# Optimization experiments

Hardware: AMD Instinct MI355X
Metric: run time of the kernel (lower is better)

## Reference

```python
import jax, jax.numpy as jnp
from jax import lax
import numpy as np

V, E, H, L = 32000, 512, 1024, 2
B, S, T = 32, 128, 128
PAD = 0


def _lstm_step(h, c, gates):
    i, f, g, o = jnp.split(gates, 4, axis=-1)
    c_new = jax.nn.sigmoid(f) * c + jax.nn.sigmoid(i) * jnp.tanh(g)
    h_new = jax.nn.sigmoid(o) * jnp.tanh(c_new)
    return h_new, c_new


def _lstm_layer(x_tbe, Wih, Whh, bih, bhh):
    # x_tbe: [T, B, in]; returns hs [T, B, H], final (h, c)
    Bn = x_tbe.shape[1]
    Hn = Whh.shape[1]
    h0 = jnp.zeros((Bn, Hn), x_tbe.dtype)
    c0 = jnp.zeros((Bn, Hn), x_tbe.dtype)

    def step(carry, x_t):
        h, c = carry
        gates = x_t @ Wih.T + h @ Whh.T + (bih + bhh)
        h, c = _lstm_step(h, c, gates)
        return (h, c), h

    (h, c), hs = lax.scan(step, (h0, c0), x_tbe)
    return hs, h, c


def setup_inputs() -> dict:
    key = jax.random.key(0)
    ks = iter(jax.random.split(key, 32))
    s = 0.02

    def p(shape):
        return (jax.random.normal(next(ks), shape, dtype=jnp.float32) * s)

    embed = p((V, E)).at[PAD].set(0.0)  # padding_idx row zeroed
    inp = {
        'src': jax.random.randint(next(ks), (B, S), 0, V),
        'tgt': jax.random.randint(next(ks), (B, T), 0, V),
        'embed': embed,
        'enc_Wih0': p((4 * H, E)), 'enc_Whh0': p((4 * H, H)),
        'enc_bih0': p((4 * H,)), 'enc_bhh0': p((4 * H,)),
        'enc_Wih1': p((4 * H, H)), 'enc_Whh1': p((4 * H, H)),
        'enc_bih1': p((4 * H,)), 'enc_bhh1': p((4 * H,)),
        'dec_Wih': p((4 * H, E + H)), 'dec_Whh': p((4 * H, H)),
        'dec_bih': p((4 * H,)), 'dec_bhh': p((4 * H,)),
        'fc_W': p((V, H)), 'fc_b': p((V,)),
    }
    return inp


def reference(src, tgt, embed, enc_Wih0, enc_Whh0, enc_bih0, enc_bhh0,
              enc_Wih1, enc_Whh1, enc_bih1, enc_bhh1,
              dec_Wih, dec_Whh, dec_bih, dec_bhh, fc_W, fc_b):
    # ----- encoder: 2-layer LSTM -----
    enc_emb = embed[src]                       # [B, S, E]
    x = jnp.transpose(enc_emb, (1, 0, 2))      # [S, B, E]
    hs0, _, _ = _lstm_layer(x, enc_Wih0, enc_Whh0, enc_bih0, enc_bhh0)
    hs1, h_last, c_last = _lstm_layer(hs0, enc_Wih1, enc_Whh1, enc_bih1, enc_bhh1)
    enc_out = jnp.transpose(hs1, (1, 0, 2))    # [B, S, H]

    # ----- decoder: attention + LSTMCell per step -----
    dec_emb = embed[tgt[:, :-1]]               # inputs for steps 1..T-1: [B, T-1, E]
    dec_xs = jnp.transpose(dec_emb, (1, 0, 2)) # [T-1, B, E]

    def dec_step(carry, x_t):
        h, c = carry
        scores = jnp.einsum('bsh,bh->bs', enc_out, h)
        w = jax.nn.softmax(scores, axis=1)
        ctx = jnp.einsum('bs,bsh->bh', w, enc_out)
        xin = jnp.concatenate([x_t, ctx], axis=1)   # [B, E+H]
        gates = xin @ dec_Wih.T + h @ dec_Whh.T + (dec_bih + dec_bhh)
        h, c = _lstm_step(h, c, gates)
        out = h @ fc_W.T + fc_b                     # [B, V]
        return (h, c), out

    _, outs = lax.scan(dec_step, (h_last, c_last), dec_xs)  # [T-1, B, V]
    return jnp.transpose(outs, (1, 0, 2))                   # [B, T-1, V]
```

## Files before the change

### kernel.cpp

```cpp
#include <hip/hip_runtime.h>

typedef unsigned short u16;
typedef __bf16 bf16x8 __attribute__((ext_vector_type(8)));
typedef float f32x4 __attribute__((ext_vector_type(4)));
typedef u16 u16x8 __attribute__((ext_vector_type(8)));
typedef unsigned u32x2 __attribute__((ext_vector_type(2)));

static_assert(sizeof(bf16x8) == 16, "bf16x8 must be 16B");

#define DEV static __device__ __forceinline__

DEV u16 f2bf(float f) {
  unsigned u = __float_as_uint(f);
  u += 0x7FFFu + ((u >> 16) & 1u);
  return (u16)(u >> 16);
}
DEV float bf2f(u16 h) { return __uint_as_float(((unsigned)h) << 16); }
DEV f32x4 mfma16(bf16x8 a, bf16x8 b, f32x4 c) {
  return __builtin_amdgcn_mfma_f32_16x16x32_bf16(a, b, c, 0, 0, 0);
}
DEV bf16x8 ldfrag(const u16* p) { return *reinterpret_cast<const bf16x8*>(p); }
DEV float sigf(float x) { return 1.0f / (1.0f + __expf(-x)); }
DEV bf16x8 asbf(f32x4 v) { union { f32x4 f; bf16x8 h; } u; u.f = v; return u.h; }
DEV void gld16(const void* g, void* l) {
  __builtin_amdgcn_global_load_lds((const __attribute__((address_space(1))) void*)g,
                                   (__attribute__((address_space(3))) void*)l, 16, 0, 0);
}

DEV void ld_a16_coh(const void* p0, const void* p1,
                    f32x4& a0, f32x4& a1, f32x4& a2, f32x4& a3,
                    f32x4& a4, f32x4& a5, f32x4& a6, f32x4& a7,
                    f32x4& b0, f32x4& b1, f32x4& b2, f32x4& b3,
                    f32x4& b4, f32x4& b5, f32x4& b6, f32x4& b7) {
  asm volatile(
      "global_load_dwordx4 %0, %16, off sc0 sc1\n\t"
      "global_load_dwordx4 %1, %16, off offset:64 sc0 sc1\n\t"
      "global_load_dwordx4 %2, %16, off offset:128 sc0 sc1\n\t"
      "global_load_dwordx4 %3, %16, off offset:192 sc0 sc1\n\t"
      "global_load_dwordx4 %4, %16, off offset:256 sc0 sc1\n\t"
      "global_load_dwordx4 %5, %16, off offset:320 sc0 sc1\n\t"
      "global_load_dwordx4 %6, %16, off offset:384 sc0 sc1\n\t"
      "global_load_dwordx4 %7, %16, off offset:448 sc0 sc1\n\t"
      "global_load_dwordx4 %8, %17, off sc0 sc1\n\t"
      "global_load_dwordx4 %9, %17, off offset:64 sc0 sc1\n\t"
      "global_load_dwordx4 %10, %17, off offset:128 sc0 sc1\n\t"
      "global_load_dwordx4 %11, %17, off offset:192 sc0 sc1\n\t"
      "global_load_dwordx4 %12, %17, off offset:256 sc0 sc1\n\t"
      "global_load_dwordx4 %13, %17, off offset:320 sc0 sc1\n\t"
      "global_load_dwordx4 %14, %17, off offset:384 sc0 sc1\n\t"
      "global_load_dwordx4 %15, %17, off offset:448 sc0 sc1\n\t"
      "s_waitcnt vmcnt(0)"
      : "=&v"(a0), "=&v"(a1), "=&v"(a2), "=&v"(a3), "=&v"(a4), "=&v"(a5), "=&v"(a6), "=&v"(a7),
        "=&v"(b0), "=&v"(b1), "=&v"(b2), "=&v"(b3), "=&v"(b4), "=&v"(b5), "=&v"(b6), "=&v"(b7)
      : "v"(p0), "v"(p1)
      : "memory");
}
DEV void ld_a16_coh_nw(const void* p0, const void* p1,
                       f32x4& a0, f32x4& a1, f32x4& a2, f32x4& a3,
                       f32x4& a4, f32x4& a5, f32x4& a6, f32x4& a7,
                       f32x4& b0, f32x4& b1, f32x4& b2, f32x4& b3,
                       f32x4& b4, f32x4& b5, f32x4& b6, f32x4& b7) {
  asm volatile(
      "global_load_dwordx4 %0, %16, off sc0 sc1\n\t"
      "global_load_dwordx4 %1, %16, off offset:64 sc0 sc1\n\t"
      "global_load_dwordx4 %2, %16, off offset:128 sc0 sc1\n\t"
      "global_load_dwordx4 %3, %16, off offset:192 sc0 sc1\n\t"
      "global_load_dwordx4 %4, %16, off offset:256 sc0 sc1\n\t"
      "global_load_dwordx4 %5, %16, off offset:320 sc0 sc1\n\t"
      "global_load_dwordx4 %6, %16, off offset:384 sc0 sc1\n\t"
      "global_load_dwordx4 %7, %16, off offset:448 sc0 sc1\n\t"
      "global_load_dwordx4 %8, %17, off sc0 sc1\n\t"
      "global_load_dwordx4 %9, %17, off offset:64 sc0 sc1\n\t"
      "global_load_dwordx4 %10, %17, off offset:128 sc0 sc1\n\t"
      "global_load_dwordx4 %11, %17, off offset:192 sc0 sc1\n\t"
      "global_load_dwordx4 %12, %17, off offset:256 sc0 sc1\n\t"
      "global_load_dwordx4 %13, %17, off offset:320 sc0 sc1\n\t"
      "global_load_dwordx4 %14, %17, off offset:384 sc0 sc1\n\t"
      "global_load_dwordx4 %15, %17, off offset:448 sc0 sc1"
      : "=&v"(a0), "=&v"(a1), "=&v"(a2), "=&v"(a3), "=&v"(a4), "=&v"(a5), "=&v"(a6), "=&v"(a7),
        "=&v"(b0), "=&v"(b1), "=&v"(b2), "=&v"(b3), "=&v"(b4), "=&v"(b5), "=&v"(b6), "=&v"(b7)
      : "v"(p0), "v"(p1)
      : "memory");
}
DEV f32x4 ld16_coh(const void* p) {
  f32x4 r;
  asm volatile("global_load_dwordx4 %0, %1, off sc0 sc1\n\ts_waitcnt vmcnt(0)"
               : "=&v"(r) : "v"(p) : "memory");
  return r;
}
DEV void ld32_coh(const void* p, f32x4& a, f32x4& b) {
  asm volatile(
      "global_load_dwordx4 %0, %2, off sc0 sc1\n\t"
      "global_load_dwordx4 %1, %2, off offset:16 sc0 sc1\n\t"
      "s_waitcnt vmcnt(0)"
      : "=&v"(a), "=&v"(b) : "v"(p) : "memory");
}
DEV void st32_coh(void* p, unsigned v) {
  asm volatile("global_store_dword %0, %1, off sc0 sc1" ::"v"(p), "v"(v) : "memory");
}
DEV void st8_coh(void* p, unsigned lo, unsigned hi) {
  u32x2 v; v[0] = lo; v[1] = hi;
  asm volatile("global_store_dwordx2 %0, %1, off sc0 sc1" ::"v"(p), "v"(v) : "memory");
}

DEV unsigned ldflag(const unsigned* p) {
  unsigned r;
  asm volatile("global_load_dword %0, %1, off sc0 sc1\n\ts_waitcnt vmcnt(0)"
               : "=&v"(r) : "v"(p) : "memory");
  return r;
}
DEV void poll128(const unsigned* fl, unsigned tgt) {
  if (tgt == 0) return;
  if (threadIdx.x < 64) {
    const unsigned* p0 = fl + (size_t)threadIdx.x * 16;
    const unsigned* p1 = fl + (size_t)(threadIdx.x + 64) * 16;
    for (;;) {
      unsigned a, b;
      asm volatile(
          "global_load_dword %0, %2, off sc0 sc1\n\t"
          "global_load_dword %1, %3, off sc0 sc1\n\t"
          "s_waitcnt vmcnt(0)"
          : "=&v"(a), "=&v"(b) : "v"(p0), "v"(p1) : "memory");
      if (__all((a >= tgt) && (b >= tgt))) break;
      __builtin_amdgcn_s_sleep(1);
    }
  }
  __syncthreads();
}
DEV void poll32(const unsigned* fl, unsigned tgt) {
  if (threadIdx.x < 64) {
    const unsigned* p0 = fl + (size_t)(threadIdx.x & 31) * 16;
    for (;;) {
      unsigned a = ldflag(p0);
      if (__all(a >= tgt)) break;
      __builtin_amdgcn_s_sleep(1);
    }
  }
  __syncthreads();
}
DEV void pollAB(const unsigned* f0, unsigned t0, const unsigned* f1, unsigned t1) {
  const bool n0 = t0 > 0, n1 = t1 > 0;
  if ((n0 || n1) && threadIdx.x < 64) {
    const unsigned* q0 = f0 + (size_t)threadIdx.x * 16;
    const unsigned* q1 = f0 + (size_t)(threadIdx.x + 64) * 16;
    const unsigned* q2 = f1 + (size_t)threadIdx.x * 16;
    const unsigned* q3 = f1 + (size_t)(threadIdx.x + 64) * 16;
    for (;;) {
      unsigned a, b, c, d;
      asm volatile(
          "global_load_dword %0, %4, off sc0 sc1\n\t"
          "global_load_dword %1, %5, off sc0 sc1\n\t"
          "global_load_dword %2, %6, off sc0 sc1\n\t"
          "global_load_dword %3, %7, off sc0 sc1\n\t"
          "s_waitcnt vmcnt(0)"
          : "=&v"(a), "=&v"(b), "=&v"(c), "=&v"(d)
          : "v"(q0), "v"(q1), "v"(q2), "v"(q3) : "memory");
      bool ok = true;
      if (n0) ok = ok && (a >= t0) && (b >= t0);
      if (n1) ok = ok && (c >= t1) && (d >= t1);
      if (__all(ok)) break;
      __builtin_amdgcn_s_sleep(1);
    }
  }
  __syncthreads();
}
DEV void setflag(unsigned* f, unsigned v) {
  asm volatile("s_waitcnt vmcnt(0)" ::: "memory");
  __syncthreads();
  if (threadIdx.x == 0) st32_coh(f, v);
}

#define Bn 32
#define Sn 128
#define Td 127
#define En 512
#define Hn 1024
#define G4 4096
#define Vn 32000

typedef u16 u16x8b __attribute__((ext_vector_type(8)));
__global__ __launch_bounds__(256) void cvt_bf16_kernel(const float* __restrict__ in,
                                                       u16* __restrict__ out, int n8) {
  int gid = blockIdx.x * 256 + threadIdx.x;
  if (gid >= n8) return;
  const float4* ip = (const float4*)in + gid * 2;
  float4 x = ip[0], y = ip[1];
  u16x8b o;
  o[0] = f2bf(x.x); o[1] = f2bf(x.y); o[2] = f2bf(x.z); o[3] = f2bf(x.w);
  o[4] = f2bf(y.x); o[5] = f2bf(y.y); o[6] = f2bf(y.z); o[7] = f2bf(y.w);
  ((u16x8b*)out)[gid] = o;
}

__global__ __launch_bounds__(256) void gather_embed_kernel(const int* __restrict__ idx, int ldidx,
                                                           const float* __restrict__ embed,
                                                           u16* __restrict__ outA, int nrows) {
  int gid = blockIdx.x * 256 + threadIdx.x;
  int total = nrows * (En / 8);
  if (gid >= total) return;
  int r = gid / (En / 8);
  int ck = gid % (En / 8);
  int tcol = r / Bn, b = r % Bn;
  int tok = idx[b * ldidx + tcol];
  const float4* src = (const float4*)(embed + (size_t)tok * En + ck * 8);
  float4 x = src[0], y = src[1];
  u16x8b o;
  o[0] = f2bf(x.x); o[1] = f2bf(x.y); o[2] = f2bf(x.z); o[3] = f2bf(x.w);
  o[4] = f2bf(y.x); o[5] = f2bf(y.y); o[6] = f2bf(y.z); o[7] = f2bf(y.w);
  *(u16x8b*)(outA + (size_t)r * En + ck * 8) = o;
}

__global__ __launch_bounds__(256) void gemm_tile_kernel(const u16* __restrict__ A, int lda,
                                                        const u16* __restrict__ W, int ldw,
                                                        const float* __restrict__ bias0,
                                                        const float* __restrict__ bias1,
                                                        float* __restrict__ Cout, int ldc,
                                                        int Mtiles, int K, int mode) {
  __shared__ u16 Asb[128 * 32];
  __shared__ u16 Bsb[128 * 32];
  int nwg = gridDim.x;
  int cpx = nwg >> 3;
  int bid = ((int)blockIdx.x & 7) * cpx + ((int)blockIdx.x >> 3);
  int mt = bid % Mtiles, nt = bid / Mtiles;
  int tid = threadIdx.x;
  int wave = tid >> 6, lane = tid & 63;
  int lrow = lane & 15, kgrp = lane >> 4;
  int wr = wave >> 1, wc = wave & 1;
  int e0 = wave * 1024 + lane * 8;
  int r0 = e0 >> 5, c0 = e0 & 31;
  int r1 = r0 + 16;
  const u16* Ab = A + (size_t)(mt * 128) * lda;
  const u16* Wb = W + (size_t)(nt * 128) * ldw;
  u16* AsW = Asb + wave * 1024;
  u16* BsW = Bsb + wave * 1024;
  f32x4 acc[4][4] = {};
  for (int k0 = 0; k0 < K; k0 += 32) {
    gld16(Ab + (size_t)r0 * lda + k0 + c0, AsW);
    gld16(Ab + (size_t)r1 * lda + k0 + c0, AsW + 512);
    gld16(Wb + (size_t)r0 * ldw + k0 + c0, BsW);
    gld16(Wb + (size_t)r1 * ldw + k0 + c0, BsW + 512);
    __syncthreads();
    bf16x8 af[4], bfr[4];
#pragma unroll
    for (int i = 0; i < 4; ++i) af[i] = ldfrag(Asb + (wr * 64 + i * 16 + lrow) * 32 + kgrp * 8);
#pragma unroll
    for (int i = 0; i < 4; ++i) bfr[i] = ldfrag(Bsb + (wc * 64 + i * 16 + lrow) * 32 + kgrp * 8);
#pragma unroll
    for (int i = 0; i < 4; ++i)
#pragma unroll
      for (int j = 0; j < 4; ++j) acc[i][j] = mfma16(af[i], bfr[j], acc[i][j]);
    __syncthreads();
  }
  if (mode == 0) {
#pragma unroll
    for (int i = 0; i < 4; ++i) {
      int m = mt * 128 + wr * 64 + i * 16 + kgrp * 4;
#pragma unroll
      for (int j = 0; j < 4; ++j) {
        int n = nt * 128 + wc * 64 + j * 16 + lrow;
        float bb = (bias0 ? bias0[n] : 0.f) + (bias1 ? bias1[n] : 0.f);
#pragma unroll
        for (int r = 0; r < 4; ++r) Cout[(size_t)(m + r) * ldc + n] = acc[i][j][r] + bb;
      }
    }
  } else {
#pragma unroll
    for (int i = 0; i < 4; ++i) {
      int m = mt * 128 + wr * 64 + i * 16 + kgrp * 4;
#pragma unroll
      for (int j = 0; j < 4; ++j) {
        int n = nt * 128 + wc * 64 + j * 16 + lrow;
        float bb = bias0[n];
#pragma unroll
        for (int r = 0; r < 4; ++r) {
          int mm = m + r;
          if (mm < Td * Bn) {
            int tt = mm >> 5, b = mm & 31;
            Cout[((size_t)b * Td + tt) * Vn + n] = acc[i][j][r] + bb;
          }
        }
      }
    }
  }
}

DEV void mm8b(const u16* __restrict__ A0, const char* __restrict__ Wl, int pitchB,
              int kByteBase, int lane, f32x4 acc[2][2]) {
  const int lrow = lane & 15, kgrp = lane >> 4;
  const char* wr0 = Wl + (size_t)lrow * pitchB;
  const char* wr1 = wr0 + (size_t)16 * pitchB;
  const int sw = (lrow & 7) << 4;
  f32x4 s0, s1, s2, s3, s4, s5, s6, s7, u0, u1, u2, u3, u4, u5, u6, u7;
  ld_a16_coh(A0 + (size_t)lrow * 1024 + kgrp * 8, A0 + (size_t)(16 + lrow) * 1024 + kgrp * 8,
             s0, s1, s2, s3, s4, s5, s6, s7, u0, u1, u2, u3, u4, u5, u6, u7);
#define KS(T, U, J, KB)                                                \
  {                                                                    \
    bf16x8 a = asbf(T);                                                \
    int kb = (KB) + (J) * 64 + kgrp * 16;                              \
    bf16x8 w0 = *(const bf16x8*)(wr0 + (size_t)(kb ^ sw));             \
    bf16x8 w1 = *(const bf16x8*)(wr1 + (size_t)(kb ^ sw));             \
    acc[0][0] = mfma16(a, w0, acc[0][0]);                              \
    acc[0][1] = mfma16(a, w1, acc[0][1]);                              \
    bf16x8 cc = asbf(U);                                               \
    acc[1][0] = mfma16(cc, w0, acc[1][0]);                             \
    acc[1][1] = mfma16(cc, w1, acc[1][1]);                             \
  }
  KS(s0, u0, 0, kByteBase) KS(s1, u1, 1, kByteBase) KS(s2, u2, 2, kByteBase)
  KS(s3, u3, 3, kByteBase) KS(s4, u4, 4, kByteBase) KS(s5, u5, 5, kByteBase)
  KS(s6, u6, 6, kByteBase) KS(s7, u7, 7, kByteBase)
}

DEV void mm8b_pair(const u16* __restrict__ A0, const char* __restrict__ Wl, int pitchB,
                   int kByteBase, int lane, f32x4 acc[2][2]) {
  const int lrow = lane & 15, kgrp = lane >> 4;
  const char* wr0 = Wl + (size_t)lrow * pitchB;
  const char* wr1 = wr0 + (size_t)16 * pitchB;
  const int sw = (lrow & 7) << 4;
  f32x4 s0, s1, s2, s3, s4, s5, s6, s7, u0, u1, u2, u3, u4, u5, u6, u7;
  f32x4 t0, t1, t2, t3, t4, t5, t6, t7, v0, v1, v2, v3, v4, v5, v6, v7;
  ld_a16_coh_nw(A0 + (size_t)lrow * 1024 + kgrp * 8, A0 + (size_t)(16 + lrow) * 1024 + kgrp * 8,
                s0, s1, s2, s3, s4, s5, s6, s7, u0, u1, u2, u3, u4, u5, u6, u7);
  ld_a16_coh(A0 + (size_t)lrow * 1024 + 256 + kgrp * 8,
             A0 + (size_t)(16 + lrow) * 1024 + 256 + kgrp * 8,
             t0, t1, t2, t3, t4, t5, t6, t7, v0, v1, v2, v3, v4, v5, v6, v7);
  __builtin_amdgcn_sched_barrier(0);
  KS(s0, u0, 0, kByteBase) KS(s1, u1, 1, kByteBase) KS(s2, u2, 2, kByteBase)
  KS(s3, u3, 3, kByteBase) KS(s4, u4, 4, kByteBase) KS(s5, u5, 5, kByteBase)
  KS(s6, u6, 6, kByteBase) KS(s7, u7, 7, kByteBase)
  KS(t0, v0, 0, kByteBase + 512) KS(t1, v1, 1, kByteBase + 512) KS(t2, v2, 2, kByteBase + 512)
  KS(t3, v3, 3, kByteBase + 512) KS(t4, v4, 4, kByteBase + 512) KS(t5, v5, 5, kByteBase + 512)
  KS(t6, v6, 6, kByteBase + 512) KS(t7, v7, 7, kByteBase + 512)
}

DEV void dump_acc(float* red, f32x4 acc[2][2], int wave, int lane) {
  int lrow = lane & 15, kgrp = lane >> 4;
#pragma unroll
  for (int m = 0; m < 2; ++m)
#pragma unroll
    for (int n = 0; n < 2; ++n)
#pragma unroll
      for (int r = 0; r < 4; ++r)
        red[((((wave * 2 + m) * 2 + n) * 16) + kgrp * 4 + r) * 16 + lrow] = acc[m][n][r];
}
DEV float rsum(const float* red, int m, int n, int rw, int l) {
  float s = 0.f;
#pragma unroll
  for (int w = 0; w < 4; ++w) s += red[((((w * 2 + m) * 2 + n) * 16) + rw) * 16 + l];
  return s;
}
DEV float lstm_apply(const float gs[4], float* c_reg) {
  float ig = sigf(gs[0]), fg = sigf(gs[1]), gg = tanhf(gs[2]), og = sigf(gs[3]);
  float cn = fg * (*c_reg) + ig * gg;
  *c_reg = cn;
  return og * tanhf(cn);
}

__global__ __launch_bounds__(256, 1) void enc_persist9(
    const float* __restrict__ premix, const u16* __restrict__ Whh0, const u16* __restrict__ Wih1,
    const u16* __restrict__ Whh1, const float* __restrict__ bih1, const float* __restrict__ bhh1,
    u16* __restrict__ h0ring, u16* __restrict__ h1ring, float* __restrict__ c1_out,
    u16* __restrict__ enc_b, unsigned* __restrict__ f0, unsigned* __restrict__ f1) {
  extern __shared__ char lds[];
  float* red = (float*)(lds + 131072);
  const int tid = threadIdx.x, wave = tid >> 6, lane = tid & 63;
  const int blk = blockIdx.x;
  const bool l1 = blk >= 128;
  const int base = (blk & 127) * 8;
  if (!l1) {
    for (int i = tid; i < 4096; i += 256) {
      int c = i >> 7;
      int kb = (i & 127) << 4;
      int row = (c >> 3) * Hn + base + (c & 7);
      f32x4 v = *(const f32x4*)(Whh0 + (size_t)row * Hn + (kb >> 1));
      *(f32x4*)(lds + c * 2048 + (kb ^ ((c & 7) << 4))) = v;
    }
  } else {
    for (int i = tid; i < 8192; i += 256) {
      int c = i >> 8;
      int kb = (i & 255) << 4;
      int row = (c >> 3) * Hn + base + (c & 7);
      const u16* src = (kb < 2048) ? (Wih1 + (size_t)row * Hn + (kb >> 1))
                                   : (Whh1 + (size_t)row * Hn + ((kb - 2048) >> 1));
      f32x4 v = *(const f32x4*)src;
      *(f32x4*)(lds + c * 4096 + (kb ^ ((c & 7) << 4))) = v;
    }
  }
  const int b_ = tid >> 3, hc = tid & 7;
  const int m = b_ >> 4, rw = b_ & 15;
  const size_t off = (size_t)b_ * Hn + base + hc;
  float c_reg = 0.f;
  __syncthreads();
  if (!l1) {
    for (int i = 0; i < Sn; ++i) {
      const float* pmr = premix + (size_t)i * (Bn * G4) + (size_t)b_ * G4 + base + hc;
      float pmv[4];
#pragma unroll
      for (int g = 0; g < 4; ++g) pmv[g] = pmr[(size_t)g * Hn];
      pollAB(f0, (unsigned)i, f1, (i >= 3) ? (unsigned)(i - 2) : 0u);
      const u16* hin = h0ring + (size_t)(i & 3) * (Bn * Hn);
      f32x4 acc[2][2] = {};
      mm8b(hin + wave * 256, lds, 2048, wave * 512, lane, acc);
      dump_acc(red, acc, wave, lane);
      __syncthreads();
      float gs[4];
#pragma unroll
      for (int g = 0; g < 4; ++g) {
        int c = g * 8 + hc;
        gs[g] = rsum(red, m, c >> 4, rw, c & 15) + pmv[g];
      }
      float hn = lstm_apply(gs, &c_reg);
      u16 mine = f2bf(hn);
      unsigned nb = (unsigned)(u16)__shfl_xor((int)mine, 1);
      if (!(tid & 1))
        st32_coh(h0ring + (size_t)((i + 1) & 3) * (Bn * Hn) + off,
                 ((unsigned)mine) | (nb << 16));
      setflag(f0 + blk * 16, (unsigned)(i + 1));
    }
  } else {
    float badd[4];
#pragma unroll
    for (int g = 0; g < 4; ++g) badd[g] = bih1[g * Hn + base + hc] + bhh1[g * Hn + base + hc];
    for (int j = 0; j < Sn; ++j) {
      pollAB(f0, (unsigned)(j + 1), f1, (unsigned)j);
      const u16* h0r = h0ring + (size_t)((j + 1) & 3) * (Bn * Hn);
      const u16* h1r = h1ring + (size_t)(j & 1) * (Bn * Hn);
      const u16* srcp = (wave < 2) ? h0r : h1r;
      int ko = (wave & 1) * 512;
      f32x4 acc[2][2] = {};
      mm8b_pair(srcp + ko, lds, 4096, wave * 1024, lane, acc);
      dump_acc(red, acc, wave, lane);
      __syncthreads();
      float gs[4];
#pragma unroll
      for (int g = 0; g < 4; ++g) {
        int c = g * 8 + hc;
        gs[g] = rsum(red, m, c >> 4, rw, c & 15) + badd[g];
      }
      float hn = lstm_apply(gs, &c_reg);
      u16 mine = f2bf(hn);
      unsigned nb = (unsigned)(u16)__shfl_xor((int)mine, 1);
      unsigned packed = ((unsigned)mine) | (nb << 16);
      if (!(tid & 1)) {
        st32_coh(h1ring + (size_t)((j + 1) & 1) * (Bn * Hn) + off, packed);
        *(unsigned*)(enc_b + (size_t)j * (Bn * Hn) + off) = packed;
      }
      if (j == Sn - 1) c1_out[off] = c_reg;
      setflag(f1 + (blk - 128) * 16, (unsigned)(j + 1));
    }
  }
}

__global__ __launch_bounds__(256, 1) void dec_persist12(
    const float* __restrict__ premix, const u16* __restrict__ Wctx, const u16* __restrict__ Whh,
    const float* __restrict__ c_init, u16* __restrict__ hbuf ,
    const u16* __restrict__ enc_b, u16* __restrict__ ctxb, u16* __restrict__ hs_dec,
    unsigned* __restrict__ fg, unsigned* __restrict__ fa) {
  extern __shared__ char lds[];
  const int tid = threadIdx.x, wave = tid >> 6, lane = tid & 63;
  const int blk = blockIdx.x;
  if (blk < 128) {
    float* red = (float*)(lds + 131072);
    const int cg = blk, base = cg * 8;
    for (int i = tid; i < 8192; i += 256) {
      int c = i >> 8;
      int kb = (i & 255) << 4;
      int row = (c >> 3) * Hn + base + (c & 7);
      const u16* src = (kb < 2048) ? (Whh + (size_t)row * Hn + (kb >> 1))
                                   : (Wctx + (size_t)row * 1536 + ((kb - 2048) >> 1));
      f32x4 v = *(const f32x4*)src;
      *(f32x4*)(lds + c * 4096 + (kb ^ ((c & 7) << 4))) = v;
    }
    const int b_ = tid >> 3, hc = tid & 7;
    const int m = b_ >> 4, rw = b_ & 15;
    const size_t off = (size_t)b_ * Hn + base + hc;
    float c_reg = c_init[off];
    __syncthreads();
    for (int t = 0; t < Td; ++t) {
      const float* pmr = premix + (size_t)t * (Bn * G4) + (size_t)b_ * G4 + base + hc;
      float pmv[4];
#pragma unroll
      for (int g = 0; g < 4; ++g) pmv[g] = pmr[(size_t)g * Hn];
      poll128(fg, (unsigned)t);
      f32x4 acc[2][2] = {};
      mm8b(hbuf + (size_t)(t & 1) * (Bn * Hn) + wave * 256, lds, 4096, wave * 512, lane, acc);
      poll32(fa, (unsigned)(t + 1));
      mm8b(ctxb + wave * 256, lds, 4096, 2048 + wave * 512, lane, acc);
      dump_acc(red, acc, wave, lane);
      __syncthreads();
      float gs[4];
#pragma unroll
      for (int g = 0; g < 4; ++g) {
        int c = g * 8 + hc;
        gs[g] = rsum(red, m, c >> 4, rw, c & 15) + pmv[g];
      }
      float hn = lstm_apply(gs, &c_reg);
      u16 mine = f2bf(hn);
      unsigned nb = (unsigned)(u16)__shfl_xor((int)mine, 1);
      unsigned packed = ((unsigned)mine) | (nb << 16);
      if (!(tid & 1)) {
        st32_coh(hbuf + (size_t)((t + 1) & 1) * (Bn * Hn) + off, packed);
        *(unsigned*)(hs_dec + (size_t)t * (Bn * Hn) + off) = packed;
      }
      setflag(fg + cg * 16, (unsigned)(t + 1));
    }
  } else {
    float* scpart = (float*)lds;
    float* scl = (float*)(lds + 33280);
    float* wsm = (float*)(lds + 33792);
    float(*cpart)[16][64] = (float(*)[16][64])(lds + 34304);
    const int b = blk - 128;
    for (int t = 0; t < Td; ++t) {
      poll128(fg, (unsigned)t);
      const u16* hb = hbuf + (size_t)(t & 1) * (Bn * Hn) + (size_t)b * Hn;
      float hf[16];
      {
        union { f32x4 f[2]; u16 u[16]; } U;
        ld32_coh(hb + lane * 16, U.f[0], U.f[1]);
#pragma unroll
        for (int k2 = 0; k2 < 16; ++k2) hf[k2] = bf2f(U.u[k2]);
      }
#pragma unroll 4
      for (int i = 0; i < 32; ++i) {
        int s = wave * 32 + i;
        const u16* er = enc_b + ((size_t)s * Bn + b) * Hn + lane * 16;
        u16x8 e0 = *(const u16x8*)er;
        u16x8 e1 = *(const u16x8*)(er + 8);
        float p2 = 0.f;
#pragma unroll
        for (int k2 = 0; k2 < 8; ++k2) p2 += bf2f(e0[k2]) * hf[k2] + bf2f(e1[k2]) * hf[8 + k2];
        scpart[s * 65 + lane] = p2;
      }
      __syncthreads();
      {
        int s2 = tid >> 1, half = tid & 1;
        const float* pp = scpart + s2 * 65 + half * 32;
        float p = 0.f;
#pragma unroll
        for (int j = 0; j < 32; ++j) p += pp[j];
        p += __shfl_xor(p, 1);
        if (half == 0) scl[s2] = p;
      }
      __syncthreads();
      if (wave == 0) {
        float sa = scl[lane], sb = scl[64 + lane];
        float mx = fmaxf(sa, sb);
#pragma unroll
        for (int o2 = 32; o2; o2 >>= 1) mx = fmaxf(mx, __shfl_xor(mx, o2));
        float ea = __expf(sa - mx), eb = __expf(sb - mx);
        float ss = ea + eb;
#pragma unroll
        for (int o2 = 32; o2; o2 >>= 1) ss += __shfl_xor(ss, o2);
        float inv = 1.0f / ss;
        wsm[lane] = ea * inv;
        wsm[64 + lane] = eb * inv;
      }
      __syncthreads();
      float a0[16];
#pragma unroll
      for (int q = 0; q < 16; ++q) a0[q] = 0.f;
      for (int i = 0; i < 32; ++i) {
        int s = wave * 32 + i;
        float w = wsm[s];
        const u16* er = enc_b + ((size_t)s * Bn + b) * Hn + lane * 16;
        u16x8 e0 = *(const u16x8*)er;
        u16x8 e1 = *(const u16x8*)(er + 8);
#pragma unroll
        for (int q = 0; q < 8; ++q) {
          a0[q] += w * bf2f(e0[q]);
          a0[8 + q] += w * bf2f(e1[q]);
        }
      }
#pragma unroll
      for (int q = 0; q < 16; ++q) cpart[wave][q][lane] = a0[q];
      __syncthreads();
      {
        unsigned pk[2];
#pragma unroll
        for (int h2 = 0; h2 < 2; ++h2) {
          float v0 = 0.f, v1 = 0.f;
          int j0 = tid * 4 + h2 * 2;
#pragma unroll
          for (int w2 = 0; w2 < 4; ++w2) {
            v0 += cpart[w2][j0 & 15][j0 >> 4];
            v1 += cpart[w2][(j0 + 1) & 15][(j0 + 1) >> 4];
          }
          pk[h2] = (unsigned)f2bf(v0) | ((unsigned)f2bf(v1) << 16);
        }
        st8_coh(ctxb + (size_t)b * Hn + tid * 4, pk[0], pk[1]);
      }
      setflag(fa + b * 16, (unsigned)(t + 1));
    }
  }
}

extern "C" void kernel_launch(void* const* d_in, const int* in_sizes, int n_in,
                              void* d_out, int out_size, void* d_ws, size_t ws_size,
                              hipStream_t stream) {
  const int* src = (const int*)d_in[0];
  const int* tgt = (const int*)d_in[1];
  const float* embed = (const float*)d_in[2];
  const float* Wih0 = (const float*)d_in[3];
  const float* Whh0 = (const float*)d_in[4];
  const float* bih0 = (const float*)d_in[5];
  const float* bhh0 = (const float*)d_in[6];
  const float* Wih1 = (const float*)d_in[7];
  const float* Whh1 = (const float*)d_in[8];
  const float* bih1 = (const float*)d_in[9];
  const float* bhh1 = (const float*)d_in[10];
  const float* dWih = (const float*)d_in[11];
  const float* dWhh = (const float*)d_in[12];
  const float* dbih = (const float*)d_in[13];
  const float* dbhh = (const float*)d_in[14];
  const float* fcW = (const float*)d_in[15];
  const float* fcb = (const float*)d_in[16];
  float* out = (float*)d_out;

  (void)hipFuncSetAttribute((const void*)enc_persist9,
                            hipFuncAttributeMaxDynamicSharedMemorySize, 147456);
  (void)hipFuncSetAttribute((const void*)dec_persist12,
                            hipFuncAttributeMaxDynamicSharedMemorySize, 147456);

  char* p = (char*)d_ws;
  auto alloc = [&](size_t bytes) {
    void* r = p;
    p += (bytes + 255) & ~(size_t)255;
    return r;
  };
  u16* Wih0_b = (u16*)alloc((size_t)G4 * En * 2);
  u16* Whh0_b = (u16*)alloc((size_t)G4 * Hn * 2);
  u16* Wih1_b = (u16*)alloc((size_t)G4 * Hn * 2);
  u16* Whh1_b = (u16*)alloc((size_t)G4 * Hn * 2);
  u16* dWih_b = (u16*)alloc((size_t)G4 * 1536 * 2);
  u16* dWhh_b = (u16*)alloc((size_t)G4 * Hn * 2);
  u16* fcW_b = (u16*)alloc((size_t)Vn * Hn * 2);
  u16* embA = (u16*)alloc((size_t)4096 * En * 2);
  float* premix = (float*)alloc((size_t)4096 * G4 * 4);
  u16* enc_b = (u16*)alloc((size_t)Sn * Bn * Hn * 2);
  u16* hs_dec = (u16*)alloc((size_t)4096 * Hn * 2);
  u16* h0ring = (u16*)alloc((size_t)4 * Bn * Hn * 2);
  u16* h1ring = (u16*)alloc((size_t)2 * Bn * Hn * 2);
  float* c1g = (float*)alloc((size_t)Bn * Hn * 4);
  u16* ctx_b = (u16*)alloc((size_t)Bn * Hn * 2);
  unsigned* counters = (unsigned*)alloc(65536);
  unsigned* flagsE0 = counters;
  unsigned* flagsE1 = counters + 2048;
  unsigned* flagsDg = counters + 4096;
  unsigned* flagsDa = counters + 6144;

  auto cvt = [&](const float* in, u16* o, size_t n) {
    int n8 = (int)(n / 8);
    cvt_bf16_kernel<<<(n8 + 255) / 256, 256, 0, stream>>>(in, o, n8);
  };
  cvt(Wih0, Wih0_b, (size_t)G4 * En);
  cvt(Whh0, Whh0_b, (size_t)G4 * Hn);
  cvt(Wih1, Wih1_b, (size_t)G4 * Hn);
  cvt(Whh1, Whh1_b, (size_t)G4 * Hn);
  cvt(dWih, dWih_b, (size_t)G4 * 1536);
  cvt(dWhh, dWhh_b, (size_t)G4 * Hn);
  cvt(fcW, fcW_b, (size_t)Vn * Hn);

  {
    int total = 4096 * (En / 8);
    gather_embed_kernel<<<(total + 255) / 256, 256, 0, stream>>>(src, Sn, embed, embA, Sn * Bn);
    gemm_tile_kernel<<<32 * 32, 256, 0, stream>>>(embA, En, Wih0_b, En, bih0, bhh0, premix, G4,
                                                  32, En, 0);
  }
  (void)hipMemsetAsync(h0ring, 0, (size_t)4 * Bn * Hn * 2, stream);
  (void)hipMemsetAsync(h1ring, 0, (size_t)2 * Bn * Hn * 2, stream);
  (void)hipMemsetAsync(counters, 0, 65536, stream);
  (void)hipMemsetAsync(hs_dec + (size_t)(Td * Bn) * Hn, 0, (size_t)(4096 - Td * Bn) * Hn * 2,
                       stream);

  enc_persist9<<<256, 256, 147456, stream>>>(premix, Whh0_b, Wih1_b, Whh1_b, bih1, bhh1, h0ring,
                                             h1ring, c1g, enc_b, flagsE0, flagsE1);

  {
    int nrows = Td * Bn;
    int total = nrows * (En / 8);
    gather_embed_kernel<<<(total + 255) / 256, 256, 0, stream>>>(tgt, Sn, embed, embA, nrows);
    gemm_tile_kernel<<<32 * 32, 256, 0, stream>>>(embA, En, dWih_b, 1536, dbih, dbhh, premix, G4,
                                                  32, En, 0);
  }

  dec_persist12<<<160, 256, 147456, stream>>>(premix, dWih_b + 512, dWhh_b, c1g,
                                              h1ring , enc_b, ctx_b, hs_dec,
                                              flagsDg, flagsDa);

  gemm_tile_kernel<<<32 * 250, 256, 0, stream>>>(hs_dec, Hn, fcW_b, Hn, fcb, nullptr, out, 0,
                                                 32, Hn, 1);
}
```

Baseline: 3.209 ms.

## Replace block-wide flag polling with per-wave polling of only needed producers

Replaces the block-level poll functions (poll128/poll32/pollAB followed by __syncthreads) with per-wave polls. Each wave now waits only on the flags of the producer blocks whose h slice it reads next. In the layer-0 encoder, the wait on layer-1 progress (ring reuse) is moved after the LSTM math, just before the h store, so it overlaps with compute. This removes block barriers and lets waves start their matmul chunks as soon as their own dependencies are ready, at the cost of subtle correctness reliance on the wave-to-producer index mapping.

```diff
diff --git a/kernel.cpp b/kernel.cpp
--- a/kernel.cpp
+++ b/kernel.cpp
@@ -109,60 +109,27 @@
                : "=&v"(r) : "v"(p) : "memory");
   return r;
 }
-DEV void poll128(const unsigned* fl, unsigned tgt) {
-  if (tgt == 0) return;
-  if (threadIdx.x < 64) {
-    const unsigned* p0 = fl + (size_t)threadIdx.x * 16;
-    const unsigned* p1 = fl + (size_t)(threadIdx.x + 64) * 16;
-    for (;;) {
-      unsigned a, b;
-      asm volatile(
-          "global_load_dword %0, %2, off sc0 sc1\n\t"
-          "global_load_dword %1, %3, off sc0 sc1\n\t"
-          "s_waitcnt vmcnt(0)"
-          : "=&v"(a), "=&v"(b) : "v"(p0), "v"(p1) : "memory");
-      if (__all((a >= tgt) && (b >= tgt))) break;
-      __builtin_amdgcn_s_sleep(1);
-    }
-  }
-  __syncthreads();
-}
-DEV void poll32(const unsigned* fl, unsigned tgt) {
-  if (threadIdx.x < 64) {
-    const unsigned* p0 = fl + (size_t)(threadIdx.x & 31) * 16;
-    for (;;) {
-      unsigned a = ldflag(p0);
-      if (__all(a >= tgt)) break;
-      __builtin_amdgcn_s_sleep(1);
-    }
-  }
-  __syncthreads();
-}
-DEV void pollAB(const unsigned* f0, unsigned t0, const unsigned* f1, unsigned t1) {
-  const bool n0 = t0 > 0, n1 = t1 > 0;
-  if ((n0 || n1) && threadIdx.x < 64) {
-    const unsigned* q0 = f0 + (size_t)threadIdx.x * 16;
-    const unsigned* q1 = f0 + (size_t)(threadIdx.x + 64) * 16;
-    const unsigned* q2 = f1 + (size_t)threadIdx.x * 16;
-    const unsigned* q3 = f1 + (size_t)(threadIdx.x + 64) * 16;
-    for (;;) {
-      unsigned a, b, c, d;
-      asm volatile(
-          "global_load_dword %0, %4, off sc0 sc1\n\t"
-          "global_load_dword %1, %5, off sc0 sc1\n\t"
-          "global_load_dword %2, %6, off sc0 sc1\n\t"
-          "global_load_dword %3, %7, off sc0 sc1\n\t"
-          "s_waitcnt vmcnt(0)"
-          : "=&v"(a), "=&v"(b), "=&v"(c), "=&v"(d)
-          : "v"(q0), "v"(q1), "v"(q2), "v"(q3) : "memory");
-      bool ok = true;
-      if (n0) ok = ok && (a >= t0) && (b >= t0);
-      if (n1) ok = ok && (c >= t1) && (d >= t1);
-      if (__all(ok)) break;
-      __builtin_amdgcn_s_sleep(1);
-    }
-  }
-  __syncthreads();
+DEV void pollWave(const unsigned* fl, int idx, unsigned tgt) {
+  const unsigned* p = fl + (size_t)idx * 16;
+  for (;;) {
+    unsigned a = ldflag(p);
+    if (__all(a >= tgt)) break;
+    __builtin_amdgcn_s_sleep(1);
+  }
+}
+DEV void pollWave2(const unsigned* fl, int i0, int i1, unsigned tgt) {
+  const unsigned* p0 = fl + (size_t)i0 * 16;
+  const unsigned* p1 = fl + (size_t)i1 * 16;
+  for (;;) {
+    unsigned a, b;
+    asm volatile(
+        "global_load_dword %0, %2, off sc0 sc1\n\t"
+        "global_load_dword %1, %3, off sc0 sc1\n\t"
+        "s_waitcnt vmcnt(0)"
+        : "=&v"(a), "=&v"(b) : "v"(p0), "v"(p1) : "memory");
+    if (__all((a >= tgt) && (b >= tgt))) break;
+    __builtin_amdgcn_s_sleep(1);
+  }
 }
 DEV void setflag(unsigned* f, unsigned v) {
   asm volatile("s_waitcnt vmcnt(0)" ::: "memory");
@@ -354,7 +321,7 @@
   return og * tanhf(cn);
 }
 
-__global__ __launch_bounds__(256, 1) void enc_persist9(
+__global__ __launch_bounds__(256, 1) void enc_persist10(
     const float* __restrict__ premix, const u16* __restrict__ Whh0, const u16* __restrict__ Wih1,
     const u16* __restrict__ Whh1, const float* __restrict__ bih1, const float* __restrict__ bhh1,
     u16* __restrict__ h0ring, u16* __restrict__ h1ring, float* __restrict__ c1_out,
@@ -390,12 +357,13 @@
   float c_reg = 0.f;
   __syncthreads();
   if (!l1) {
+    const int widx = wave * 32 + (lane & 31);
     for (int i = 0; i < Sn; ++i) {
       const float* pmr = premix + (size_t)i * (Bn * G4) + (size_t)b_ * G4 + base + hc;
       float pmv[4];
 #pragma unroll
       for (int g = 0; g < 4; ++g) pmv[g] = pmr[(size_t)g * Hn];
-      pollAB(f0, (unsigned)i, f1, (i >= 3) ? (unsigned)(i - 2) : 0u);
+      if (i) pollWave(f0, widx, (unsigned)i);
       const u16* hin = h0ring + (size_t)(i & 3) * (Bn * Hn);
       f32x4 acc[2][2] = {};
       mm8b(hin + wave * 256, lds, 2048, wave * 512, lane, acc);
@@ -408,6 +376,7 @@
         gs[g] = rsum(red, m, c >> 4, rw, c & 15) + pmv[g];
       }
       float hn = lstm_apply(gs, &c_reg);
+      if (i >= 3) pollWave2(f1, lane, 64 + lane, (unsigned)(i - 2));
       u16 mine = f2bf(hn);
       unsigned nb = (unsigned)(u16)__shfl_xor((int)mine, 1);
       if (!(tid & 1))
@@ -420,7 +389,8 @@
 #pragma unroll
     for (int g = 0; g < 4; ++g) badd[g] = bih1[g * Hn + base + hc] + bhh1[g * Hn + base + hc];
     for (int j = 0; j < Sn; ++j) {
-      pollAB(f0, (unsigned)(j + 1), f1, (unsigned)j);
+      if (wave < 2) pollWave(f0, wave * 64 + lane, (unsigned)(j + 1));
+      else if (j >= 1) pollWave(f1, (wave - 2) * 64 + lane, (unsigned)j);
       const u16* h0r = h0ring + (size_t)((j + 1) & 3) * (Bn * Hn);
       const u16* h1r = h1ring + (size_t)(j & 1) * (Bn * Hn);
       const u16* srcp = (wave < 2) ? h0r : h1r;
@@ -449,7 +419,7 @@
   }
 }
 
-__global__ __launch_bounds__(256, 1) void dec_persist12(
+__global__ __launch_bounds__(256, 1) void dec_persist13(
     const float* __restrict__ premix, const u16* __restrict__ Wctx, const u16* __restrict__ Whh,
     const float* __restrict__ c_init, u16* __restrict__ hbuf ,
     const u16* __restrict__ enc_b, u16* __restrict__ ctxb, u16* __restrict__ hs_dec,
@@ -472,6 +442,7 @@
     const int b_ = tid >> 3, hc = tid & 7;
     const int m = b_ >> 4, rw = b_ & 15;
     const size_t off = (size_t)b_ * Hn + base + hc;
+    const int widx = wave * 32 + (lane & 31);
     float c_reg = c_init[off];
     __syncthreads();
     for (int t = 0; t < Td; ++t) {
@@ -479,10 +450,10 @@
       float pmv[4];
 #pragma unroll
       for (int g = 0; g < 4; ++g) pmv[g] = pmr[(size_t)g * Hn];
-      poll128(fg, (unsigned)t);
+      if (t) pollWave(fg, widx, (unsigned)t);
       f32x4 acc[2][2] = {};
       mm8b(hbuf + (size_t)(t & 1) * (Bn * Hn) + wave * 256, lds, 4096, wave * 512, lane, acc);
-      poll32(fa, (unsigned)(t + 1));
+      pollWave(fa, lane & 31, (unsigned)(t + 1));
       mm8b(ctxb + wave * 256, lds, 4096, 2048 + wave * 512, lane, acc);
       dump_acc(red, acc, wave, lane);
       __syncthreads();
@@ -509,7 +480,7 @@
     float(*cpart)[16][64] = (float(*)[16][64])(lds + 34304);
     const int b = blk - 128;
     for (int t = 0; t < Td; ++t) {
-      poll128(fg, (unsigned)t);
+      if (t) pollWave2(fg, lane, 64 + lane, (unsigned)t);
       const u16* hb = hbuf + (size_t)(t & 1) * (Bn * Hn) + (size_t)b * Hn;
       float hf[16];
       {
@@ -614,9 +585,9 @@
   const float* fcb = (const float*)d_in[16];
   float* out = (float*)d_out;
 
-  (void)hipFuncSetAttribute((const void*)enc_persist9,
+  (void)hipFuncSetAttribute((const void*)enc_persist10,
                             hipFuncAttributeMaxDynamicSharedMemorySize, 147456);
-  (void)hipFuncSetAttribute((const void*)dec_persist12,
+  (void)hipFuncSetAttribute((const void*)dec_persist13,
                             hipFuncAttributeMaxDynamicSharedMemorySize, 147456);
 
   char* p = (char*)d_ws;
@@ -670,8 +641,8 @@
   (void)hipMemsetAsync(hs_dec + (size_t)(Td * Bn) * Hn, 0, (size_t)(4096 - Td * Bn) * Hn * 2,
                        stream);
 
-  enc_persist9<<<256, 256, 147456, stream>>>(premix, Whh0_b, Wih1_b, Whh1_b, bih1, bhh1, h0ring,
-                                             h1ring, c1g, enc_b, flagsE0, flagsE1);
+  enc_persist10<<<256, 256, 147456, stream>>>(premix, Whh0_b, Wih1_b, Whh1_b, bih1, bhh1, h0ring,
+                                              h1ring, c1g, enc_b, flagsE0, flagsE1);
 
   {
     int nrows = Td * Bn;
@@ -681,7 +652,7 @@
                                                   32, En, 0);
   }
 
-  dec_persist12<<<160, 256, 147456, stream>>>(premix, dWih_b + 512, dWhh_b, c1g,
+  dec_persist13<<<160, 256, 147456, stream>>>(premix, dWih_b + 512, dWhh_b, c1g,
                                               h1ring , enc_b, ctx_b, hs_dec,
                                               flagsDg, flagsDa);
 
```

Result: no change. 3.255 ms (+1.4%).
